# Optimization experiments

Measured on AMD Instinct MI355X. Metric: run time of the kernel, lower is better.

Reference implementation:

```python
import jax, jax.numpy as jnp
import numpy as np

NX, NY, NZ = 64, 48, 32          # grid_resolution
N = NX * NY * NZ                 # 98304 grid cells
P = 10                           # neighbors_in_radius
D = 3                            # spatial dims
M = 5                            # num_modes (fourier)
BN = 64                          # base_neurons
BN_IN = 8                        # base_neurons_in (output channels)
IN_FEAT = D * (1 + 2 * M)        # 33


def _linear_init(k, fan_in, fan_out):
    s = 1.0 / np.sqrt(fan_in)
    kw, kb = jax.random.split(k)
    W = jax.random.uniform(kw, (fan_in, fan_out), jnp.float32, -s, s)
    b = jax.random.uniform(kb, (fan_out,), jnp.float32, -s, s)
    return W, b


def setup_inputs() -> dict:
    key = jax.random.key(0)
    ks = jax.random.split(key, 6)
    # neighbor point coordinates gathered by ball query: (b, N, P, 3)
    x = jax.random.normal(ks[0], (1, N, P, D), jnp.float32)
    # regular grid coordinates: (b, nx, ny, nz, 3)
    grid = jax.random.normal(ks[1], (1, NX, NY, NZ, D), jnp.float32)
    # fourier frequency buffer: exp(linspace(0, pi, num_modes))
    freqs = jnp.exp(jnp.linspace(0.0, float(np.pi), M)).astype(jnp.float32)
    W1, b1 = _linear_init(ks[2], IN_FEAT, BN)
    W2, b2 = _linear_init(ks[3], BN, BN // 2)
    W3, b3 = _linear_init(ks[4], BN // 2, BN_IN)
    return dict(x=x, grid=grid, freqs=freqs,
                W1=W1, b1=b1, W2=W2, b2=b2, W3=W3, b3=b3)


def _fourier_encode(coords, freqs):
    # coords: (b, N, P, D), freqs: (F,)
    scaled = coords[..., None, :] * freqs[:, None]          # (b, N, P, F, D)
    b, n, p = coords.shape[:3]
    scaled = scaled.reshape(b, n, p, -1)                    # (b, N, P, F*D)
    return jnp.concatenate([jnp.sin(scaled), jnp.cos(scaled)], axis=-1)


def reference(x, grid, freqs, W1, b1, W2, b2, W3, b3):
    gelu = lambda t: jax.nn.gelu(t, approximate=False)  # torch F.gelu default = exact erf
    # Fourier feature encode neighbor coords: (b, N, P, 33)
    facets = jnp.concatenate([x, _fourier_encode(x, freqs)], axis=-1)
    h = gelu(facets @ W1 + b1)                              # (b, N, P, 64)
    h = gelu(h @ W2 + b2)                                   # (b, N, P, 32)
    h = jnp.tanh(h @ W3 + b3)                               # (b, N, P, 8)
    # mask out padded neighbors (zero coords); original uses x-coordinate channel
    mask = (jnp.abs(x[..., 0:1]) > 1e-6).astype(h.dtype)    # (b, N, P, 1)
    out = jnp.sum(h * mask, axis=2)                         # scatter/aggregate -> (b, N, 8)
    out = out.reshape(out.shape[0], NX, NY, NZ, BN_IN)
    return jnp.transpose(out, (0, 4, 1, 2, 3))              # (b, 8, nx, ny, nz)
```

## Files before the change

### kernel.cpp

```cpp
#include <hip/hip_runtime.h>
#include <math.h>

#define NXD 64
#define NYD 48
#define NZD 32
#define NPT (NXD*NYD*NZD)
#define PN  10
#define MF  5
#define H1  64
#define H2  32
#define H3  8

#define PTS_PER_BLOCK 32
#define ROWS_PER_BLOCK (PTS_PER_BLOCK*PN)
#define TILES_PER_WAVE 5

#define A2S 72
#define A3S 40

typedef __attribute__((ext_vector_type(8))) short short8;
typedef __attribute__((ext_vector_type(4))) float f32x4;

__device__ __forceinline__ short f2bf(float f) {
    unsigned u = __float_as_uint(f);
    unsigned r = (u + 0x7fffu + ((u >> 16) & 1u)) >> 16;
    return (short)r;
}

__device__ __forceinline__ unsigned short f2bf_hu(float f) {
    return (unsigned short)((__float_as_uint(f) + 0x8000u) >> 16);
}

__device__ __forceinline__ unsigned pack2_bf16(float lo, float hi) {
    return __builtin_amdgcn_perm(__float_as_uint(hi) + 0x8000u,
                                 __float_as_uint(lo) + 0x8000u, 0x07060302u);
}

__device__ __forceinline__ float gelu_fast(float x) {
    float x2 = x * x;
    float t  = x * (1.59576912f + 0.07135482f * x2);
    float E  = __expf(t);
    return x - x * __builtin_amdgcn_rcpf(E + 1.0f);
}

__device__ __forceinline__ float tanh_fast(float v) {
    float E = __expf(2.0f * v);
    return 1.0f - 2.0f * __builtin_amdgcn_rcpf(E + 1.0f);
}

__global__ __launch_bounds__(256) void domino_mfma_kernel(
    const float* __restrict__ x,
    const float* __restrict__ freqs,
    const float* __restrict__ W1,
    const float* __restrict__ b1,
    const float* __restrict__ W2,
    const float* __restrict__ b2,
    const float* __restrict__ W3,
    const float* __restrict__ b3,
    float* __restrict__ out)
{
    __shared__ float obuf[ROWS_PER_BLOCK * 9];
    __shared__ __align__(16) unsigned short a2buf[4][16 * A2S];
    __shared__ __align__(16) unsigned short a3buf[4][16 * A3S];
    __shared__ __align__(16) float mcx[4][16];
    __shared__ __align__(16) float mv32[4][16];

    const int tid  = threadIdx.x;
    const int w    = tid >> 6;
    const int lane = tid & 63;
    const int lr   = lane & 15;
    const int lg   = lane >> 4;

    float fr[MF];
    #pragma unroll
    for (int m = 0; m < MF; ++m) fr[m] = freqs[m];

    short8 B1f[4];
    float  w32[4], bv1[4];
    #pragma unroll
    for (int t1 = 0; t1 < 4; ++t1) {
        #pragma unroll
        for (int j = 0; j < 8; ++j)
            B1f[t1][j] = f2bf(W1[(lg*8 + j)*H1 + t1*16 + lr]);
        w32[t1] = W1[32*H1 + t1*16 + lr];
        bv1[t1] = b1[t1*16 + lr];
    }
    short8 B2f[2][2];
    float  bv2[2];
    #pragma unroll
    for (int s = 0; s < 2; ++s)
        #pragma unroll
        for (int t2 = 0; t2 < 2; ++t2)
            #pragma unroll
            for (int j = 0; j < 8; ++j)
                B2f[s][t2][j] = f2bf(W2[(s*32 + lg*8 + j)*H2 + t2*16 + lr]);
    #pragma unroll
    for (int t2 = 0; t2 < 2; ++t2) bv2[t2] = b2[t2*16 + lr];

    short8 B3f;
    float  bv3 = (lr < H3) ? b3[lr] : 0.0f;
    #pragma unroll
    for (int j = 0; j < 8; ++j)
        B3f[j] = (lr < H3) ? f2bf(W3[(lg*8 + j)*H3 + lr]) : (short)0;

    const int wrow0 = blockIdx.x * ROWS_PER_BLOCK + w * (TILES_PER_WAVE*16);

    #pragma unroll 1
    for (int t = 0; t < TILES_PER_WAVE; ++t) {
        const int myrow = wrow0 + t*16 + lr;

        const float* xp = x + (size_t)myrow * 3;
        const float cx = xp[0], cy = xp[1], cz = xp[2];

        float sv[15], cv[15];
        #pragma unroll
        for (int m = 0; m < MF; ++m) {
            __sincosf(fr[m]*cx, &sv[m*3+0], &cv[m*3+0]);
            __sincosf(fr[m]*cy, &sv[m*3+1], &cv[m*3+1]);
            __sincosf(fr[m]*cz, &sv[m*3+2], &cv[m*3+2]);
        }

        if (lg == 0) { mcx[w][lr] = cx; mv32[w][lr] = cv[14]; }

        float fv[8];
        if (lg == 0) {
            fv[0]=cx; fv[1]=cy; fv[2]=cz;
            fv[3]=sv[0]; fv[4]=sv[1]; fv[5]=sv[2]; fv[6]=sv[3]; fv[7]=sv[4];
        } else if (lg == 1) {
            fv[0]=sv[5];  fv[1]=sv[6];  fv[2]=sv[7];  fv[3]=sv[8];
            fv[4]=sv[9];  fv[5]=sv[10]; fv[6]=sv[11]; fv[7]=sv[12];
        } else if (lg == 2) {
            fv[0]=sv[13]; fv[1]=sv[14]; fv[2]=cv[0];  fv[3]=cv[1];
            fv[4]=cv[2];  fv[5]=cv[3];  fv[6]=cv[4];  fv[7]=cv[5];
        } else {
            fv[0]=cv[6];  fv[1]=cv[7];  fv[2]=cv[8];  fv[3]=cv[9];
            fv[4]=cv[10]; fv[5]=cv[11]; fv[6]=cv[12]; fv[7]=cv[13];
        }
        union { unsigned u[4]; short8 s8; } a1u;
        #pragma unroll
        for (int j = 0; j < 4; ++j) a1u.u[j] = pack2_bf16(fv[2*j], fv[2*j+1]);
        const short8 a1 = a1u.s8;

        f32x4 c1[4];
        #pragma unroll
        for (int t1 = 0; t1 < 4; ++t1) {
            f32x4 ci = {bv1[t1], bv1[t1], bv1[t1], bv1[t1]};
            c1[t1] = __builtin_amdgcn_mfma_f32_16x16x32_bf16(a1, B1f[t1], ci, 0, 0, 0);
        }
        const f32x4 v32r = *(const f32x4*)&mv32[w][lg*4];
        const f32x4 mxr  = *(const f32x4*)&mcx[w][lg*4];
        #pragma unroll
        for (int t1 = 0; t1 < 4; ++t1)
            #pragma unroll
            for (int r = 0; r < 4; ++r)
                c1[t1][r] += v32r[r] * w32[t1];
        #pragma unroll
        for (int t1 = 0; t1 < 4; ++t1)
            #pragma unroll
            for (int r = 0; r < 4; ++r)
                c1[t1][r] = gelu_fast(c1[t1][r]);

        #pragma unroll
        for (int t1 = 0; t1 < 4; ++t1)
            #pragma unroll
            for (int r = 0; r < 4; ++r)
                a2buf[w][(lg*4 + r)*A2S + t1*16 + lr] = f2bf_hu(c1[t1][r]);
        short8 a2f[2];
        #pragma unroll
        for (int s = 0; s < 2; ++s)
            a2f[s] = *(const short8*)&a2buf[w][lr*A2S + s*32 + lg*8];

        f32x4 c2[2];
        #pragma unroll
        for (int t2 = 0; t2 < 2; ++t2) {
            f32x4 ci = {bv2[t2], bv2[t2], bv2[t2], bv2[t2]};
            ci = __builtin_amdgcn_mfma_f32_16x16x32_bf16(a2f[0], B2f[0][t2], ci, 0, 0, 0);
            c2[t2] = __builtin_amdgcn_mfma_f32_16x16x32_bf16(a2f[1], B2f[1][t2], ci, 0, 0, 0);
        }
        #pragma unroll
        for (int t2 = 0; t2 < 2; ++t2)
            #pragma unroll
            for (int r = 0; r < 4; ++r)
                c2[t2][r] = gelu_fast(c2[t2][r]);

        #pragma unroll
        for (int t2 = 0; t2 < 2; ++t2)
            #pragma unroll
            for (int r = 0; r < 4; ++r)
                a3buf[w][(lg*4 + r)*A3S + t2*16 + lr] = f2bf_hu(c2[t2][r]);
        short8 a3f = *(const short8*)&a3buf[w][lr*A3S + lg*8];

        f32x4 c3 = {bv3, bv3, bv3, bv3};
        c3 = __builtin_amdgcn_mfma_f32_16x16x32_bf16(a3f, B3f, c3, 0, 0, 0);

        #pragma unroll
        for (int r = 0; r < 4; ++r) {
            const int brow = w*(TILES_PER_WAVE*16) + t*16 + lg*4 + r;
            const float mk = (fabsf(mxr[r]) > 1e-6f) ? 1.0f : 0.0f;
            if (lr < H3) obuf[brow*9 + lr] = mk * tanh_fast(c3[r]);
        }
    }

    __syncthreads();

    {
        const int p  = tid >> 3;
        const int ch = tid & 7;
        float sum = 0.0f;
        #pragma unroll
        for (int i = 0; i < PN; ++i) sum += obuf[(p*PN + i)*9 + ch];
        const int gp = blockIdx.x * PTS_PER_BLOCK + p;
        out[(size_t)ch * NPT + gp] = sum;
    }
}

extern "C" void kernel_launch(void* const* d_in, const int* in_sizes, int n_in,
                              void* d_out, int out_size, void* d_ws, size_t ws_size,
                              hipStream_t stream) {
    const float* x     = (const float*)d_in[0];
    const float* freqs = (const float*)d_in[2];
    const float* W1    = (const float*)d_in[3];
    const float* b1    = (const float*)d_in[4];
    const float* W2    = (const float*)d_in[5];
    const float* b2    = (const float*)d_in[6];
    const float* W3    = (const float*)d_in[7];
    const float* b3    = (const float*)d_in[8];
    float* out = (float*)d_out;

    const int grid = NPT / PTS_PER_BLOCK;
    domino_mfma_kernel<<<grid, 256, 0, stream>>>(x, freqs, W1, b1, W2, b2, W3, b3, out);
}
```

Measured before the change: 127.6 us.

## Distribute Fourier sincos across lanes and build layer-1 operand via LDS

Previously every lane computed all 15 sin/cos pairs for its row, and three quarters of those were thrown away. Now each lane computes one (mode, dim) sin/cos for four rows, using the hardware fract/sin/cos instructions on revolution-scaled inputs. The results are written to a new per-wave LDS A-operand buffer and read back as a short8 fragment. GELU and tanh are rewritten with exp2 and FMA forms. The final reduction lane mapping is swapped so global stores are coalesced per channel. The cost is extra LDS traffic and a cross-lane dependence on LDS writes without an explicit barrier, relying on wave-level execution.

```diff
diff --git a/kernel.cpp b/kernel.cpp
--- a/kernel.cpp
+++ b/kernel.cpp
@@ -15,37 +15,40 @@
 #define ROWS_PER_BLOCK (PTS_PER_BLOCK*PN)
 #define TILES_PER_WAVE 5
 
+#define A1S 40
 #define A2S 72
 #define A3S 40
 
 typedef __attribute__((ext_vector_type(8))) short short8;
 typedef __attribute__((ext_vector_type(4))) float f32x4;
+
+extern "C" __device__ float __ocml_exp2_f32(float);
 
 __device__ __forceinline__ short f2bf(float f) {
     unsigned u = __float_as_uint(f);
     unsigned r = (u + 0x7fffu + ((u >> 16) & 1u)) >> 16;
     return (short)r;
 }
-
 __device__ __forceinline__ unsigned short f2bf_hu(float f) {
     return (unsigned short)((__float_as_uint(f) + 0x8000u) >> 16);
 }
 
-__device__ __forceinline__ unsigned pack2_bf16(float lo, float hi) {
-    return __builtin_amdgcn_perm(__float_as_uint(hi) + 0x8000u,
-                                 __float_as_uint(lo) + 0x8000u, 0x07060302u);
-}
-
 __device__ __forceinline__ float gelu_fast(float x) {
     float x2 = x * x;
-    float t  = x * (1.59576912f + 0.07135482f * x2);
-    float E  = __expf(t);
-    return x - x * __builtin_amdgcn_rcpf(E + 1.0f);
-}
-
+    float p  = __builtin_fmaf(-0.07135482f, x2, -1.59576912f);
+    float s  = x * p;
+    float E  = __ocml_exp2_f32(s * 1.44269504f);
+    return x * __builtin_amdgcn_rcpf(E + 1.0f);
+}
 __device__ __forceinline__ float tanh_fast(float v) {
-    float E = __expf(2.0f * v);
-    return 1.0f - 2.0f * __builtin_amdgcn_rcpf(E + 1.0f);
+    float E = __ocml_exp2_f32(v * -2.88539008f);
+    float r = __builtin_amdgcn_rcpf(E + 1.0f);
+    return __builtin_fmaf(2.0f, r, -1.0f);
+}
+__device__ __forceinline__ void sincos_rev(float r, float* s, float* c) {
+    float f = __builtin_amdgcn_fractf(r);
+    *s = __builtin_amdgcn_sinf(f);
+    *c = __builtin_amdgcn_cosf(f);
 }
 
 __global__ __launch_bounds__(256) void domino_mfma_kernel(
@@ -60,6 +63,7 @@
     float* __restrict__ out)
 {
     __shared__ float obuf[ROWS_PER_BLOCK * 9];
+    __shared__ __align__(16) unsigned short a1buf[4][16 * A1S];
     __shared__ __align__(16) unsigned short a2buf[4][16 * A2S];
     __shared__ __align__(16) unsigned short a3buf[4][16 * A3S];
     __shared__ __align__(16) float mcx[4][16];
@@ -71,9 +75,11 @@
     const int lr   = lane & 15;
     const int lg   = lane >> 4;
 
-    float fr[MF];
-    #pragma unroll
-    for (int m = 0; m < MF; ++m) fr[m] = freqs[m];
+    const int sc_m = (lr < 15) ? (lr / 3) : 4;
+    const int sc_d = lr % 3;
+    const float scale_rev = freqs[sc_m] * 0.15915494309189535f;
+    const int st_row = lane / 3;
+    const int st_d   = lane % 3;
 
     short8 B1f[4];
     float  w32[4], bv1[4];
@@ -107,39 +113,27 @@
 
     #pragma unroll 1
     for (int t = 0; t < TILES_PER_WAVE; ++t) {
-        const int myrow = wrow0 + t*16 + lr;
-
-        const float* xp = x + (size_t)myrow * 3;
-        const float cx = xp[0], cy = xp[1], cz = xp[2];
-
-        float sv[15], cv[15];
-        #pragma unroll
-        for (int m = 0; m < MF; ++m) {
-            __sincosf(fr[m]*cx, &sv[m*3+0], &cv[m*3+0]);
-            __sincosf(fr[m]*cy, &sv[m*3+1], &cv[m*3+1]);
-            __sincosf(fr[m]*cz, &sv[m*3+2], &cv[m*3+2]);
-        }
-
-        if (lg == 0) { mcx[w][lr] = cx; mv32[w][lr] = cv[14]; }
-
-        float fv[8];
-        if (lg == 0) {
-            fv[0]=cx; fv[1]=cy; fv[2]=cz;
-            fv[3]=sv[0]; fv[4]=sv[1]; fv[5]=sv[2]; fv[6]=sv[3]; fv[7]=sv[4];
-        } else if (lg == 1) {
-            fv[0]=sv[5];  fv[1]=sv[6];  fv[2]=sv[7];  fv[3]=sv[8];
-            fv[4]=sv[9];  fv[5]=sv[10]; fv[6]=sv[11]; fv[7]=sv[12];
-        } else if (lg == 2) {
-            fv[0]=sv[13]; fv[1]=sv[14]; fv[2]=cv[0];  fv[3]=cv[1];
-            fv[4]=cv[2];  fv[5]=cv[3];  fv[6]=cv[4];  fv[7]=cv[5];
-        } else {
-            fv[0]=cv[6];  fv[1]=cv[7];  fv[2]=cv[8];  fv[3]=cv[9];
-            fv[4]=cv[10]; fv[5]=cv[11]; fv[6]=cv[12]; fv[7]=cv[13];
-        }
-        union { unsigned u[4]; short8 s8; } a1u;
-        #pragma unroll
-        for (int j = 0; j < 4; ++j) a1u.u[j] = pack2_bf16(fv[2*j], fv[2*j+1]);
-        const short8 a1 = a1u.s8;
+        const int row0 = wrow0 + t*16;
+
+        if (lane < 48) {
+            const float c = x[(size_t)(row0 + st_row)*3 + st_d];
+            a1buf[w][st_row*A1S + st_d] = f2bf_hu(c);
+            if (st_d == 0) mcx[w][st_row] = c;
+        }
+        if (lr < 15) {
+            #pragma unroll
+            for (int i = 0; i < 4; ++i) {
+                const int rr = lg + 4*i;
+                const float c = x[(size_t)(row0 + rr)*3 + sc_d];
+                float s, co;
+                sincos_rev(scale_rev * c, &s, &co);
+                a1buf[w][rr*A1S + 3  + lr] = f2bf_hu(s);
+                a1buf[w][rr*A1S + 18 + lr] = f2bf_hu(co);
+                if (lr == 14) mv32[w][rr] = co;
+            }
+        }
+
+        const short8 a1 = *(const short8*)&a1buf[w][lr*A1S + lg*8];
 
         f32x4 c1[4];
         #pragma unroll
@@ -153,7 +147,7 @@
         for (int t1 = 0; t1 < 4; ++t1)
             #pragma unroll
             for (int r = 0; r < 4; ++r)
-                c1[t1][r] += v32r[r] * w32[t1];
+                c1[t1][r] = __builtin_fmaf(v32r[r], w32[t1], c1[t1][r]);
         #pragma unroll
         for (int t1 = 0; t1 < 4; ++t1)
             #pragma unroll
@@ -188,7 +182,7 @@
             #pragma unroll
             for (int r = 0; r < 4; ++r)
                 a3buf[w][(lg*4 + r)*A3S + t2*16 + lr] = f2bf_hu(c2[t2][r]);
-        short8 a3f = *(const short8*)&a3buf[w][lr*A3S + lg*8];
+        const short8 a3f = *(const short8*)&a3buf[w][lr*A3S + lg*8];
 
         f32x4 c3 = {bv3, bv3, bv3, bv3};
         c3 = __builtin_amdgcn_mfma_f32_16x16x32_bf16(a3f, B3f, c3, 0, 0, 0);
@@ -204,8 +198,8 @@
     __syncthreads();
 
     {
-        const int p  = tid >> 3;
-        const int ch = tid & 7;
+        const int p  = tid & 31;
+        const int ch = tid >> 5;
         float sum = 0.0f;
         #pragma unroll
         for (int i = 0; i < PN; ++i) sum += obuf[(p*PN + i)*9 + ch];
```

After: 143.2 us. 1.12x slower.

## Compute only per-lane Fourier features with hardware sin and exp2-based activations

Applied to the files above, without the earlier changes.

Each lane now evaluates only the 8 Fourier features it feeds into the MFMA A-fragment, using v_fract plus the hardware sin instruction on pre-scaled frequencies (cos via a quarter-turn phase), instead of all 30 sincos values per lane. GELU and tanh are rewritten with exp2 and folded constants to save a few ops. The layer-3 staging buffer reuses the layer-2 buffer to cut LDS, and the final reduction remaps threads so global stores are coalesced per channel. The changes reduce transcendental work and LDS footprint but rely on hardware sin accuracy and on in-wave ordering for the shared buffer reuse.

```diff
diff --git a/kernel.cpp b/kernel.cpp
--- a/kernel.cpp
+++ b/kernel.cpp
@@ -21,16 +21,16 @@
 typedef __attribute__((ext_vector_type(8))) short short8;
 typedef __attribute__((ext_vector_type(4))) float f32x4;
 
+extern "C" __device__ float __ocml_exp2_f32(float);
+
 __device__ __forceinline__ short f2bf(float f) {
     unsigned u = __float_as_uint(f);
     unsigned r = (u + 0x7fffu + ((u >> 16) & 1u)) >> 16;
     return (short)r;
 }
-
 __device__ __forceinline__ unsigned short f2bf_hu(float f) {
     return (unsigned short)((__float_as_uint(f) + 0x8000u) >> 16);
 }
-
 __device__ __forceinline__ unsigned pack2_bf16(float lo, float hi) {
     return __builtin_amdgcn_perm(__float_as_uint(hi) + 0x8000u,
                                  __float_as_uint(lo) + 0x8000u, 0x07060302u);
@@ -38,14 +38,14 @@
 
 __device__ __forceinline__ float gelu_fast(float x) {
     float x2 = x * x;
-    float t  = x * (1.59576912f + 0.07135482f * x2);
-    float E  = __expf(t);
-    return x - x * __builtin_amdgcn_rcpf(E + 1.0f);
-}
-
+    float p  = __builtin_fmaf(-0.10294296f, x2, -2.30220846f);
+    float E  = __ocml_exp2_f32(x * p);
+    return x * __builtin_amdgcn_rcpf(E + 1.0f);
+}
 __device__ __forceinline__ float tanh_fast(float v) {
-    float E = __expf(2.0f * v);
-    return 1.0f - 2.0f * __builtin_amdgcn_rcpf(E + 1.0f);
+    float E = __ocml_exp2_f32(v * -2.88539008f);
+    float r = __builtin_amdgcn_rcpf(E + 1.0f);
+    return __builtin_fmaf(2.0f, r, -1.0f);
 }
 
 __global__ __launch_bounds__(256) void domino_mfma_kernel(
@@ -61,7 +61,6 @@
 {
     __shared__ float obuf[ROWS_PER_BLOCK * 9];
     __shared__ __align__(16) unsigned short a2buf[4][16 * A2S];
-    __shared__ __align__(16) unsigned short a3buf[4][16 * A3S];
     __shared__ __align__(16) float mcx[4][16];
     __shared__ __align__(16) float mv32[4][16];
 
@@ -71,9 +70,31 @@
     const int lr   = lane & 15;
     const int lg   = lane >> 4;
 
-    float fr[MF];
-    #pragma unroll
-    for (int m = 0; m < MF; ++m) fr[m] = freqs[m];
+    float frv[MF];
+    #pragma unroll
+    for (int m = 0; m < MF; ++m) frv[m] = freqs[m] * 0.15915494309189535f;
+    float sc[8], ph[8];
+    int   djv[8];
+    bool  rawv[8];
+    {
+        const int k0 = lg * 8;
+        #pragma unroll
+        for (int j = 0; j < 8; ++j) {
+            const int  kk    = k0 + j;
+            const bool raw   = (kk < 3);
+            const bool isCos = (kk >= 18);
+            int idx = isCos ? (kk - 18) : (kk - 3);
+            if (raw) idx = 0;
+            const int m = idx / 3;
+            const int d = idx - m * 3;
+            float f = (m == 0) ? frv[0] : (m == 1) ? frv[1] : (m == 2) ? frv[2]
+                      : (m == 3) ? frv[3] : frv[4];
+            sc[j]   = raw ? 0.0f : f;
+            ph[j]   = isCos ? 0.25f : 0.0f;
+            djv[j]  = raw ? kk : d;
+            rawv[j] = raw;
+        }
+    }
 
     short8 B1f[4];
     float  w32[4], bv1[4];
@@ -112,29 +133,19 @@
         const float* xp = x + (size_t)myrow * 3;
         const float cx = xp[0], cy = xp[1], cz = xp[2];
 
-        float sv[15], cv[15];
-        #pragma unroll
-        for (int m = 0; m < MF; ++m) {
-            __sincosf(fr[m]*cx, &sv[m*3+0], &cv[m*3+0]);
-            __sincosf(fr[m]*cy, &sv[m*3+1], &cv[m*3+1]);
-            __sincosf(fr[m]*cz, &sv[m*3+2], &cv[m*3+2]);
-        }
-
-        if (lg == 0) { mcx[w][lr] = cx; mv32[w][lr] = cv[14]; }
+        if (lg == 0) {
+            mcx[w][lr] = cx;
+            float f = __builtin_amdgcn_fractf(__builtin_fmaf(frv[4], cz, 0.25f));
+            mv32[w][lr] = __builtin_amdgcn_sinf(f);
+        }
 
         float fv[8];
-        if (lg == 0) {
-            fv[0]=cx; fv[1]=cy; fv[2]=cz;
-            fv[3]=sv[0]; fv[4]=sv[1]; fv[5]=sv[2]; fv[6]=sv[3]; fv[7]=sv[4];
-        } else if (lg == 1) {
-            fv[0]=sv[5];  fv[1]=sv[6];  fv[2]=sv[7];  fv[3]=sv[8];
-            fv[4]=sv[9];  fv[5]=sv[10]; fv[6]=sv[11]; fv[7]=sv[12];
-        } else if (lg == 2) {
-            fv[0]=sv[13]; fv[1]=sv[14]; fv[2]=cv[0];  fv[3]=cv[1];
-            fv[4]=cv[2];  fv[5]=cv[3];  fv[6]=cv[4];  fv[7]=cv[5];
-        } else {
-            fv[0]=cv[6];  fv[1]=cv[7];  fv[2]=cv[8];  fv[3]=cv[9];
-            fv[4]=cv[10]; fv[5]=cv[11]; fv[6]=cv[12]; fv[7]=cv[13];
+        #pragma unroll
+        for (int j = 0; j < 8; ++j) {
+            const float c = (djv[j] == 0) ? cx : ((djv[j] == 1) ? cy : cz);
+            const float f = __builtin_amdgcn_fractf(__builtin_fmaf(sc[j], c, ph[j]));
+            const float v = __builtin_amdgcn_sinf(f);
+            fv[j] = rawv[j] ? c : v;
         }
         union { unsigned u[4]; short8 s8; } a1u;
         #pragma unroll
@@ -153,7 +164,7 @@
         for (int t1 = 0; t1 < 4; ++t1)
             #pragma unroll
             for (int r = 0; r < 4; ++r)
-                c1[t1][r] += v32r[r] * w32[t1];
+                c1[t1][r] = __builtin_fmaf(v32r[r], w32[t1], c1[t1][r]);
         #pragma unroll
         for (int t1 = 0; t1 < 4; ++t1)
             #pragma unroll
@@ -183,12 +194,13 @@
             for (int r = 0; r < 4; ++r)
                 c2[t2][r] = gelu_fast(c2[t2][r]);
 
+        unsigned short* a3p = &a2buf[w][0];
         #pragma unroll
         for (int t2 = 0; t2 < 2; ++t2)
             #pragma unroll
             for (int r = 0; r < 4; ++r)
-                a3buf[w][(lg*4 + r)*A3S + t2*16 + lr] = f2bf_hu(c2[t2][r]);
-        short8 a3f = *(const short8*)&a3buf[w][lr*A3S + lg*8];
+                a3p[(lg*4 + r)*A3S + t2*16 + lr] = f2bf_hu(c2[t2][r]);
+        const short8 a3f = *(const short8*)&a3p[lr*A3S + lg*8];
 
         f32x4 c3 = {bv3, bv3, bv3, bv3};
         c3 = __builtin_amdgcn_mfma_f32_16x16x32_bf16(a3f, B3f, c3, 0, 0, 0);
@@ -204,8 +216,8 @@
     __syncthreads();
 
     {
-        const int p  = tid >> 3;
-        const int ch = tid & 7;
+        const int p  = tid & 31;
+        const int ch = tid >> 5;
         float sum = 0.0f;
         #pragma unroll
         for (int i = 0; i < PN; ++i) sum += obuf[(p*PN + i)*9 + ch];
```

New measurement: 140.4 us. 10.0% more time.

## Batch GELU/tanh reciprocals across quads and reuse a2buf for layer-3 staging

Applied to the files above, without the earlier changes.

GELU and tanh are rewritten to use exp2 with prescaled constants and a single shared reciprocal per group of four values. Each group is computed via product tricks, cutting transcendental rcp instructions from four to one. The layer-3 staging buffer is aliased onto a2buf to save LDS. The output reduction mapping is changed so consecutive threads write consecutive points, giving coalesced global stores. Risks include overflow of the four-way product, which the clamp at 30 only partly guards against, plus some precision loss.

```diff
diff --git a/kernel.cpp b/kernel.cpp
--- a/kernel.cpp
+++ b/kernel.cpp
@@ -21,31 +21,60 @@
 typedef __attribute__((ext_vector_type(8))) short short8;
 typedef __attribute__((ext_vector_type(4))) float f32x4;
 
+extern "C" __device__ float __ocml_exp2_f32(float);
+
 __device__ __forceinline__ short f2bf(float f) {
     unsigned u = __float_as_uint(f);
     unsigned r = (u + 0x7fffu + ((u >> 16) & 1u)) >> 16;
     return (short)r;
 }
-
 __device__ __forceinline__ unsigned short f2bf_hu(float f) {
     return (unsigned short)((__float_as_uint(f) + 0x8000u) >> 16);
 }
-
 __device__ __forceinline__ unsigned pack2_bf16(float lo, float hi) {
     return __builtin_amdgcn_perm(__float_as_uint(hi) + 0x8000u,
                                  __float_as_uint(lo) + 0x8000u, 0x07060302u);
 }
 
-__device__ __forceinline__ float gelu_fast(float x) {
-    float x2 = x * x;
-    float t  = x * (1.59576912f + 0.07135482f * x2);
-    float E  = __expf(t);
-    return x - x * __builtin_amdgcn_rcpf(E + 1.0f);
-}
-
-__device__ __forceinline__ float tanh_fast(float v) {
-    float E = __expf(2.0f * v);
-    return 1.0f - 2.0f * __builtin_amdgcn_rcpf(E + 1.0f);
+__device__ __forceinline__ f32x4 gelu_quad(f32x4 v) {
+    f32x4 D;
+    #pragma unroll
+    for (int r = 0; r < 4; ++r) {
+        float x2 = v[r] * v[r];
+        float p  = __builtin_fmaf(-0.10294296f, x2, -2.30220846f);
+        float t  = fminf(v[r] * p, 30.0f);
+        D[r] = __ocml_exp2_f32(t) + 1.0f;
+    }
+    float q0  = D[0] * D[1];
+    float q1  = D[2] * D[3];
+    float R   = __builtin_amdgcn_rcpf(q0 * q1);
+    float q1R = q1 * R;
+    float q0R = q0 * R;
+    f32x4 g;
+    g[0] = v[0] * (D[1] * q1R);
+    g[1] = v[1] * (D[0] * q1R);
+    g[2] = v[2] * (D[3] * q0R);
+    g[3] = v[3] * (D[2] * q0R);
+    return g;
+}
+__device__ __forceinline__ f32x4 tanh_quad(f32x4 v) {
+    f32x4 D;
+    #pragma unroll
+    for (int r = 0; r < 4; ++r) {
+        float t = fminf(v[r] * -2.88539008f, 30.0f);
+        D[r] = __ocml_exp2_f32(t) + 1.0f;
+    }
+    float q0  = D[0] * D[1];
+    float q1  = D[2] * D[3];
+    float R   = __builtin_amdgcn_rcpf(q0 * q1);
+    float q1R = q1 * R;
+    float q0R = q0 * R;
+    f32x4 o;
+    o[0] = __builtin_fmaf(2.0f, D[1] * q1R, -1.0f);
+    o[1] = __builtin_fmaf(2.0f, D[0] * q1R, -1.0f);
+    o[2] = __builtin_fmaf(2.0f, D[3] * q0R, -1.0f);
+    o[3] = __builtin_fmaf(2.0f, D[2] * q0R, -1.0f);
+    return o;
 }
 
 __global__ __launch_bounds__(256) void domino_mfma_kernel(
@@ -61,7 +90,6 @@
 {
     __shared__ float obuf[ROWS_PER_BLOCK * 9];
     __shared__ __align__(16) unsigned short a2buf[4][16 * A2S];
-    __shared__ __align__(16) unsigned short a3buf[4][16 * A3S];
     __shared__ __align__(16) float mcx[4][16];
     __shared__ __align__(16) float mv32[4][16];
 
@@ -153,12 +181,10 @@
         for (int t1 = 0; t1 < 4; ++t1)
             #pragma unroll
             for (int r = 0; r < 4; ++r)
-                c1[t1][r] += v32r[r] * w32[t1];
+                c1[t1][r] = __builtin_fmaf(v32r[r], w32[t1], c1[t1][r]);
         #pragma unroll
         for (int t1 = 0; t1 < 4; ++t1)
-            #pragma unroll
-            for (int r = 0; r < 4; ++r)
-                c1[t1][r] = gelu_fast(c1[t1][r]);
+            c1[t1] = gelu_quad(c1[t1]);
 
         #pragma unroll
         for (int t1 = 0; t1 < 4; ++t1)
@@ -179,33 +205,33 @@
         }
         #pragma unroll
         for (int t2 = 0; t2 < 2; ++t2)
+            c2[t2] = gelu_quad(c2[t2]);
+
+        unsigned short* a3p = &a2buf[w][0];
+        #pragma unroll
+        for (int t2 = 0; t2 < 2; ++t2)
             #pragma unroll
             for (int r = 0; r < 4; ++r)
-                c2[t2][r] = gelu_fast(c2[t2][r]);
-
-        #pragma unroll
-        for (int t2 = 0; t2 < 2; ++t2)
-            #pragma unroll
-            for (int r = 0; r < 4; ++r)
-                a3buf[w][(lg*4 + r)*A3S + t2*16 + lr] = f2bf_hu(c2[t2][r]);
-        short8 a3f = *(const short8*)&a3buf[w][lr*A3S + lg*8];
+                a3p[(lg*4 + r)*A3S + t2*16 + lr] = f2bf_hu(c2[t2][r]);
+        const short8 a3f = *(const short8*)&a3p[lr*A3S + lg*8];
 
         f32x4 c3 = {bv3, bv3, bv3, bv3};
         c3 = __builtin_amdgcn_mfma_f32_16x16x32_bf16(a3f, B3f, c3, 0, 0, 0);
 
+        const f32x4 th = tanh_quad(c3);
         #pragma unroll
         for (int r = 0; r < 4; ++r) {
             const int brow = w*(TILES_PER_WAVE*16) + t*16 + lg*4 + r;
             const float mk = (fabsf(mxr[r]) > 1e-6f) ? 1.0f : 0.0f;
-            if (lr < H3) obuf[brow*9 + lr] = mk * tanh_fast(c3[r]);
+            if (lr < H3) obuf[brow*9 + lr] = mk * th[r];
         }
     }
 
     __syncthreads();
 
     {
-        const int p  = tid >> 3;
-        const int ch = tid & 7;
+        const int p  = tid & 31;
+        const int ch = tid >> 5;
         float sum = 0.0f;
         #pragma unroll
         for (int i = 0; i < PN; ++i) sum += obuf[(p*PN + i)*9 + ch];
```

Result: slower. 140.5 us (+10.2%).
